# Optimization experiments

Hardware: AMD Instinct MI355X
Metric: run time of the kernel (lower is better)

## Reference

```python
import jax, jax.numpy as jnp
import numpy as np

N_POINTS = 1 << 20
N_LEVELS = 16
F_PER_LVL = 2
LOG2_T = 19
T = 1 << LOG2_T
BASE_RES = 16
PER_LEVEL_SCALE = float(np.exp2(np.log2(2048.0 / 16.0) / (N_LEVELS - 1)))
# 8 trilinear corner offsets [8,3]
OFFSETS = np.stack(np.meshgrid(*([np.array([0, 1])] * 3), indexing='ij'), axis=-1).reshape(8, 3)
PRIMES = np.array([1, 2654435761, 805459861], dtype=np.uint32)  # tcnn spatial hash primes


def _level_params(l):
    # tcnn: grid_scale = 2^(l*log2(s)) * base - 1 ; resolution = ceil(scale)+1
    scale = np.exp2(l * np.log2(PER_LEVEL_SCALE)) * BASE_RES - 1.0
    res = int(np.ceil(scale)) + 1
    return float(scale), res


def hash_encode(x, table):
    """x: [N,3] in [0,1]; table: [L,T,F]. Returns [N, L*F]."""
    offs = jnp.asarray(OFFSETS)                     # [8,3] int32
    primes = jnp.asarray(PRIMES)                    # [3] uint32
    feats = []
    for l in range(N_LEVELS):
        scale, res = _level_params(l)
        pos = x * scale + 0.5                       # [N,3]
        pos_grid = jnp.floor(pos)
        w = pos - pos_grid                          # [N,3] interp weights
        c0 = pos_grid.astype(jnp.int32)             # [N,3]
        corners = c0[None, :, :] + offs[:, None, :]  # [8,N,3]
        if res ** 3 <= T:
            # dense indexing for coarse levels (fits in hashmap)
            cc = jnp.clip(corners, 0, res - 1)
            idx = cc[..., 0] + cc[..., 1] * res + cc[..., 2] * (res * res)
        else:
            cu = corners.astype(jnp.uint32)
            h = (cu[..., 0] * primes[0]) ^ (cu[..., 1] * primes[1]) ^ (cu[..., 2] * primes[2])
            idx = (h & jnp.uint32(T - 1)).astype(jnp.int32)
        f = table[l][idx]                           # [8,N,F] gather
        # trilinear weights: prod over dims of (w if corner bit else 1-w)
        wc = jnp.prod(jnp.where(offs[:, None, :] == 1, w[None], 1.0 - w[None]), axis=-1)  # [8,N]
        feats.append(jnp.sum(wc[..., None] * f, axis=0))  # [N,F]
    return jnp.concatenate(feats, axis=-1)          # [N, 32]


def _softplus10(z):
    return jax.nn.softplus(10.0 * z) / 10.0


def setup_inputs() -> dict:
    key = jax.random.key(0)
    k = jax.random.split(key, 6)
    x = jax.random.uniform(k[0], (N_POINTS, 3), dtype=jnp.float32)
    table = jax.random.normal(k[1], (N_LEVELS, T, F_PER_LVL), dtype=jnp.float32) * 1e-2
    w1 = jax.random.normal(k[2], (64, 32), dtype=jnp.float32) * 0.1
    w2 = jax.random.normal(k[3], (64, 64), dtype=jnp.float32) * 0.1
    w3 = jax.random.normal(k[4], (64, 64), dtype=jnp.float32) * 0.1
    w4 = jax.random.normal(k[5], (1, 64), dtype=jnp.float32) * 0.1
    return {"x": x, "table": table, "w1": w1, "w2": w2, "w3": w3, "w4": w4}


def reference(x, table, w1, w2, w3, w4):
    enc = hash_encode(x, table)                     # [N,32]
    h = _softplus10(enc @ w1.T)
    h = _softplus10(h @ w2.T)
    h = _softplus10(h @ w3.T)
    sdf = h @ w4.T                                  # [N,1]
    return sdf
```

## Files before the change

kernel.cpp:

```cpp
#include <hip/hip_runtime.h>
#include <cmath>

#define T_SIZE (1u << 19)

typedef _Float16 h8 __attribute__((ext_vector_type(8)));
typedef _Float16 h4 __attribute__((ext_vector_type(4)));
typedef _Float16 h2 __attribute__((ext_vector_type(2)));
typedef float f4 __attribute__((ext_vector_type(4)));

struct Levels {
    float scale[16];
    int   res[16];
    unsigned dense_mask;
};

__device__ __forceinline__ float softplus10(float z) {
    float e = __builtin_amdgcn_exp2f(fminf(z * 14.426950408889634f, 126.0f));
    return __builtin_amdgcn_logf(1.0f + e) * 0.069314718055994531f;
}

__global__ __launch_bounds__(256) void convert_table_kernel(
    const float2* __restrict__ t, h2* __restrict__ o, int total4)
{
    int i = blockIdx.x * 256 + threadIdx.x;
    if (i >= total4) return;
    const float2* src = t + (size_t)i * 4;
    h8 r;
#pragma unroll
    for (int j = 0; j < 4; ++j) {
        float2 v = src[j];
        r[2 * j]     = (_Float16)v.x;
        r[2 * j + 1] = (_Float16)v.y;
    }
    *(h8*)(o + (size_t)i * 4) = r;
}

__global__ __launch_bounds__(256) void encode_kernel(
    const float* __restrict__ xs, const h2* __restrict__ table,
    h2* __restrict__ enc2, Levels lv, int N)
{
    __shared__ float sx[768];
    __shared__ float s_scale[16];
    __shared__ int   s_res[16];

    const int i0 = blockIdx.x * 256;
    for (int t = threadIdx.x; t < 768; t += 256) sx[t] = xs[(size_t)i0 * 3 + t];
    if (threadIdx.x < 16) {
        s_scale[threadIdx.x] = lv.scale[threadIdx.x];
        s_res[threadIdx.x]   = lv.res[threadIdx.x];
    }
    __syncthreads();

    const int l = blockIdx.y;
    const int i = i0 + threadIdx.x;
    if (i >= N) return;

    const float px = sx[threadIdx.x * 3 + 0];
    const float py = sx[threadIdx.x * 3 + 1];
    const float pz = sx[threadIdx.x * 3 + 2];
    const float s  = s_scale[l];
    const int  res = s_res[l];

    float fx = px * s + 0.5f, fy = py * s + 0.5f, fz = pz * s + 0.5f;
    float gx = floorf(fx), gy = floorf(fy), gz = floorf(fz);
    float wx = fx - gx, wy = fy - gy, wz = fz - gz;
    int cx = (int)gx, cy = (int)gy, cz = (int)gz;

    const h2* tl = table + (size_t)l * T_SIZE;
    float2 vx0[4], vx1[4];

    if ((lv.dense_mask >> l) & 1u) {
        int r1 = res - 1;
        int x0 = min(cx, r1), x1 = min(cx + 1, r1);
        int y0 = min(cy, r1), y1 = min(cy + 1, r1);
        int z0 = min(cz, r1), z1 = min(cz + 1, r1);
        int rr = res * res;
        int bases[4] = {y0 * res + z0 * rr, y0 * res + z1 * rr,
                        y1 * res + z0 * rr, y1 * res + z1 * rr};
#pragma unroll
        for (int j = 0; j < 4; ++j) {
            int idx0 = x0 + bases[j];
            int idx1 = x1 + bases[j];
            h4 pr = *(const h4*)(tl + (idx0 & ~1));
            float2 lo = make_float2((float)pr[0], (float)pr[1]);
            float2 hi = make_float2((float)pr[2], (float)pr[3]);
            bool hi0 = idx0 & 1;
            vx0[j] = hi0 ? hi : lo;
            if (hi0 && idx1 != idx0) {
                h2 v = tl[idx1];
                vx1[j] = make_float2((float)v[0], (float)v[1]);
            } else {
                vx1[j] = (idx1 == idx0) ? vx0[j] : hi;
            }
        }
    } else {
        unsigned hy0 = (unsigned)cy * 2654435761u, hy1 = (unsigned)(cy + 1) * 2654435761u;
        unsigned hz0 = (unsigned)cz * 805459861u,  hz1 = (unsigned)(cz + 1) * 805459861u;
        unsigned Y[4] = {hy0 ^ hz0, hy0 ^ hz1, hy1 ^ hz0, hy1 ^ hz1};
        const bool odd = (cx & 1);
        const unsigned M = T_SIZE - 1;
#pragma unroll
        for (int j = 0; j < 4; ++j) {
            unsigned h0m = ((unsigned)cx ^ Y[j]) & M;
            unsigned h1m = ((unsigned)(cx + 1) ^ Y[j]) & M;
            h4 pr = *(const h4*)(tl + (h0m & ~1u));
            float2 lo = make_float2((float)pr[0], (float)pr[1]);
            float2 hi = make_float2((float)pr[2], (float)pr[3]);
            bool h0hi = (h0m & 1u);
            vx0[j] = h0hi ? hi : lo;
            if (odd) {
                h2 v = tl[h1m];
                vx1[j] = make_float2((float)v[0], (float)v[1]);
            } else {
                vx1[j] = h0hi ? lo : hi;
            }
        }
    }

    float wx0 = 1.f - wx, wy0 = 1.f - wy, wz0 = 1.f - wz;
    float wyz[4] = {wy0 * wz0, wy0 * wz, wy * wz0, wy * wz};
    float f0 = 0.f, f1 = 0.f;
#pragma unroll
    for (int j = 0; j < 4; ++j) {
        float w0 = wx0 * wyz[j], w1 = wx * wyz[j];
        f0 += w0 * vx0[j].x + w1 * vx1[j].x;
        f1 += w0 * vx0[j].y + w1 * vx1[j].y;
    }

    h2 r;
    r[0] = (_Float16)f0;
    r[1] = (_Float16)f1;
    enc2[(size_t)l * N + i] = r;
}

__global__ __launch_bounds__(256, 3) void mlp_kernel(
    const h2* __restrict__ enc2,
    const float* __restrict__ w1, const float* __restrict__ w2,
    const float* __restrict__ w3, const float* __restrict__ w4,
    float* __restrict__ out, int nTiles, int N)
{
    constexpr int AR = 72;
    __shared__ __align__(16) _Float16 sAct[256 * AR];

    const int tid = threadIdx.x;
    const int wave = tid >> 6;
    const int lane = tid & 63;
    const int lrow = lane & 15;
    const int quad = lane >> 4;
    const int waveRow = wave * 64;
    const f4 zero = {0.f, 0.f, 0.f, 0.f};

    h8 aW1[4];
#pragma unroll
    for (int tm = 0; tm < 4; ++tm) {
        const float* src = w1 + (tm * 16 + lrow) * 32 + quad * 8;
#pragma unroll
        for (int j = 0; j < 8; ++j) aW1[tm][j] = (_Float16)src[j];
    }
    h8 aW2[4][2], aW3[4][2];
#pragma unroll
    for (int tm = 0; tm < 4; ++tm)
#pragma unroll
        for (int km = 0; km < 2; ++km) {
            const float* s2 = w2 + (tm * 16 + lrow) * 64 + km * 32 + quad * 8;
            const float* s3 = w3 + (tm * 16 + lrow) * 64 + km * 32 + quad * 8;
#pragma unroll
            for (int j = 0; j < 8; ++j) {
                aW2[tm][km][j] = (_Float16)s2[j];
                aW3[tm][km][j] = (_Float16)s3[j];
            }
        }
    float w4f[16];
#pragma unroll
    for (int tm = 0; tm < 4; ++tm)
#pragma unroll
        for (int r = 0; r < 4; ++r)
            w4f[tm * 4 + r] = w4[tm * 16 + quad * 4 + r];

    for (int tile = blockIdx.x; tile < nTiles; tile += gridDim.x) {
        const int blockPt = tile * 256;

#pragma unroll
        for (int t = 0; t < 4; ++t) {
            const int ptg = blockPt + waveRow + t * 16 + lrow;
            h8 b;
#pragma unroll
            for (int d = 0; d < 4; ++d) {
                h2 p = enc2[(size_t)(quad * 4 + d) * N + ptg];
                b[2 * d]     = p[0];
                b[2 * d + 1] = p[1];
            }
            const int arow = (waveRow + t * 16 + lrow) * AR;
#pragma unroll
            for (int tm = 0; tm < 4; ++tm) {
                f4 acc = __builtin_amdgcn_mfma_f32_16x16x32_f16(aW1[tm], b, zero, 0, 0, 0);
                h4 pk;
#pragma unroll
                for (int r = 0; r < 4; ++r) pk[r] = (_Float16)softplus10(acc[r]);
                *(h4*)&sAct[arow + tm * 16 + quad * 4] = pk;
            }
        }

#pragma unroll
        for (int t = 0; t < 4; ++t) {
            const int arow = (waveRow + t * 16 + lrow) * AR;
            h8 b0 = *(const h8*)&sAct[arow + quad * 8];
            h8 b1 = *(const h8*)&sAct[arow + 32 + quad * 8];
            f4 accs[4];
#pragma unroll
            for (int tm = 0; tm < 4; ++tm) {
                f4 acc = __builtin_amdgcn_mfma_f32_16x16x32_f16(aW2[tm][0], b0, zero, 0, 0, 0);
                acc     = __builtin_amdgcn_mfma_f32_16x16x32_f16(aW2[tm][1], b1, acc,  0, 0, 0);
                accs[tm] = acc;
            }
#pragma unroll
            for (int tm = 0; tm < 4; ++tm) {
                h4 pk;
#pragma unroll
                for (int r = 0; r < 4; ++r) pk[r] = (_Float16)softplus10(accs[tm][r]);
                *(h4*)&sAct[arow + tm * 16 + quad * 4] = pk;
            }
        }

#pragma unroll
        for (int t = 0; t < 4; ++t) {
            const int arow = (waveRow + t * 16 + lrow) * AR;
            h8 b0 = *(const h8*)&sAct[arow + quad * 8];
            h8 b1 = *(const h8*)&sAct[arow + 32 + quad * 8];
            float sum = 0.f;
#pragma unroll
            for (int tm = 0; tm < 4; ++tm) {
                f4 acc = __builtin_amdgcn_mfma_f32_16x16x32_f16(aW3[tm][0], b0, zero, 0, 0, 0);
                acc     = __builtin_amdgcn_mfma_f32_16x16x32_f16(aW3[tm][1], b1, acc,  0, 0, 0);
#pragma unroll
                for (int r = 0; r < 4; ++r)
                    sum += w4f[tm * 4 + r] * softplus10(acc[r]);
            }
            sum += __shfl_xor(sum, 16, 64);
            sum += __shfl_xor(sum, 32, 64);
            if (quad == 0)
                out[blockPt + waveRow + t * 16 + lrow] = sum;
        }
    }
}

__global__ __launch_bounds__(256) void encode_kernel_f32(
    const float* __restrict__ xs, const float2* __restrict__ table,
    h2* __restrict__ enc2, Levels lv, int N)
{
    const int i = blockIdx.x * 256 + threadIdx.x;
    const int l = blockIdx.y;
    if (i >= N) return;
    float px = xs[3 * i], py = xs[3 * i + 1], pz = xs[3 * i + 2];
    float s = lv.scale[l];
    int res = lv.res[l];
    float fx = px * s + 0.5f, fy = py * s + 0.5f, fz = pz * s + 0.5f;
    float gx = floorf(fx), gy = floorf(fy), gz = floorf(fz);
    float wx = fx - gx, wy = fy - gy, wz = fz - gz;
    int cx = (int)gx, cy = (int)gy, cz = (int)gz;
    unsigned idx[8];
    if ((lv.dense_mask >> l) & 1u) {
        int r1 = res - 1;
        int x0 = min(cx, r1), x1 = min(cx + 1, r1);
        int y0 = min(cy, r1), y1 = min(cy + 1, r1);
        int z0 = min(cz, r1), z1 = min(cz + 1, r1);
        int rr = res * res;
        idx[0] = x0 + y0 * res + z0 * rr; idx[1] = x0 + y0 * res + z1 * rr;
        idx[2] = x0 + y1 * res + z0 * rr; idx[3] = x0 + y1 * res + z1 * rr;
        idx[4] = x1 + y0 * res + z0 * rr; idx[5] = x1 + y0 * res + z1 * rr;
        idx[6] = x1 + y1 * res + z0 * rr; idx[7] = x1 + y1 * res + z1 * rr;
    } else {
        unsigned hx0 = (unsigned)cx, hx1 = (unsigned)(cx + 1);
        unsigned hy0 = (unsigned)cy * 2654435761u, hy1 = (unsigned)(cy + 1) * 2654435761u;
        unsigned hz0 = (unsigned)cz * 805459861u,  hz1 = (unsigned)(cz + 1) * 805459861u;
        idx[0] = (hx0^hy0^hz0) & (T_SIZE-1); idx[1] = (hx0^hy0^hz1) & (T_SIZE-1);
        idx[2] = (hx0^hy1^hz0) & (T_SIZE-1); idx[3] = (hx0^hy1^hz1) & (T_SIZE-1);
        idx[4] = (hx1^hy0^hz0) & (T_SIZE-1); idx[5] = (hx1^hy0^hz1) & (T_SIZE-1);
        idx[6] = (hx1^hy1^hz0) & (T_SIZE-1); idx[7] = (hx1^hy1^hz1) & (T_SIZE-1);
    }
    const float2* tl = table + (size_t)l * T_SIZE;
    float wx0 = 1.f - wx, wy0 = 1.f - wy, wz0 = 1.f - wz;
    float wcs[8] = {wx0*wy0*wz0, wx0*wy0*wz, wx0*wy*wz0, wx0*wy*wz,
                    wx*wy0*wz0,  wx*wy0*wz,  wx*wy*wz0,  wx*wy*wz};
    float f0 = 0.f, f1 = 0.f;
#pragma unroll
    for (int c = 0; c < 8; ++c) {
        float2 v = tl[idx[c]];
        f0 += wcs[c] * v.x; f1 += wcs[c] * v.y;
    }
    h2 r; r[0] = (_Float16)f0; r[1] = (_Float16)f1;
    enc2[(size_t)l * N + i] = r;
}

extern "C" void kernel_launch(void* const* d_in, const int* in_sizes, int n_in,
                              void* d_out, int out_size, void* d_ws, size_t ws_size,
                              hipStream_t stream) {
    const float* x     = (const float*)d_in[0];
    const float* table = (const float*)d_in[1];
    const float* w1    = (const float*)d_in[2];
    const float* w2    = (const float*)d_in[3];
    const float* w3    = (const float*)d_in[4];
    const float* w4    = (const float*)d_in[5];
    float* out = (float*)d_out;
    const int N = in_sizes[0] / 3;

    Levels lv;
    lv.dense_mask = 0;
    const double pls = exp2(log2(2048.0 / 16.0) / 15.0);
    const double lg  = log2(pls);
    for (int l = 0; l < 16; ++l) {
        double sc = exp2((double)l * lg) * 16.0 - 1.0;
        int res = (int)ceil(sc) + 1;
        lv.scale[l] = (float)sc;
        lv.res[l]   = res;
        if ((long long)res * res * res <= (long long)T_SIZE) lv.dense_mask |= (1u << l);
    }

    const size_t encBytes   = (size_t)16 * N * 4;
    const size_t tableBytes = (size_t)16 * T_SIZE * 4;
    h2* enc2 = (h2*)d_ws;

    const int ptBlocks = (N + 255) / 256;
    dim3 encGrid(ptBlocks, 16);

    if (ws_size >= encBytes + tableBytes) {
        h2* table16 = (h2*)((char*)d_ws + encBytes);
        const int total4 = 16 * T_SIZE / 4;
        hipLaunchKernelGGL(convert_table_kernel, dim3((total4 + 255) / 256), dim3(256), 0,
                           stream, (const float2*)table, table16, total4);
        hipLaunchKernelGGL(encode_kernel, encGrid, dim3(256), 0, stream,
                           x, (const h2*)table16, enc2, lv, N);
    } else {
        hipLaunchKernelGGL(encode_kernel_f32, encGrid, dim3(256), 0, stream,
                           x, (const float2*)table, enc2, lv, N);
    }

    const int nTiles = N / 256;
    const int mlpBlocks = 768;
    hipLaunchKernelGGL(mlp_kernel, dim3(mlpBlocks), dim3(256), 0, stream,
                       enc2, w1, w2, w3, w4, out, nTiles, N);
}
```

Baseline: 537.2 us.

## Interleave encoding by level groups, preconvert MLP weights to fp16, raise occupancy

The encoding buffer changes from level-major h2 to groups of four levels packed into 16-byte records per point. Each MLP lane now fetches its B fragment with a single 16-byte load instead of four strided 4-byte loads. A small kernel converts w1-w3 to fp16 once per call. The MLP kernel reloads W2 and W3 fragments inside its loop so fewer registers stay live, which allows launch bounds of 4 blocks per CU, and it switches from a grid-stride loop to fixed groups of 4 tiles per block. This assumes N is a multiple of 1024 and adds one extra launch plus repeated weight loads from cache.

```diff
diff --git a/kernel.cpp b/kernel.cpp
--- a/kernel.cpp
+++ b/kernel.cpp
@@ -35,9 +35,21 @@
     *(h8*)(o + (size_t)i * 4) = r;
 }
 
+__global__ __launch_bounds__(256) void convert_weights_kernel(
+    const float* __restrict__ w1, const float* __restrict__ w2,
+    const float* __restrict__ w3, _Float16* __restrict__ o)
+{
+    int i = blockIdx.x * 256 + threadIdx.x;
+    float v;
+    if (i < 2048)      v = w1[i];
+    else if (i < 6144) v = w2[i - 2048];
+    else               v = w3[i - 6144];
+    o[i] = (_Float16)v;
+}
+
 __global__ __launch_bounds__(256) void encode_kernel(
     const float* __restrict__ xs, const h2* __restrict__ table,
-    h2* __restrict__ enc2, Levels lv, int N)
+    char* __restrict__ enc3, Levels lv, int N)
 {
     __shared__ float sx[768];
     __shared__ float s_scale[16];
@@ -130,14 +142,27 @@
     h2 r;
     r[0] = (_Float16)f0;
     r[1] = (_Float16)f1;
-    enc2[(size_t)l * N + i] = r;
-}
-
-__global__ __launch_bounds__(256, 3) void mlp_kernel(
-    const h2* __restrict__ enc2,
-    const float* __restrict__ w1, const float* __restrict__ w2,
-    const float* __restrict__ w3, const float* __restrict__ w4,
-    float* __restrict__ out, int nTiles, int N)
+    *(h2*)(enc3 + (((size_t)(l >> 2) * N + i) << 4) + ((l & 3) << 2)) = r;
+}
+
+template <typename WT>
+__device__ __forceinline__ h8 load_frag8(const WT* p) {
+    if constexpr (sizeof(WT) == 2) {
+        return *(const h8*)p;
+    } else {
+        h8 r;
+#pragma unroll
+        for (int j = 0; j < 8; ++j) r[j] = (_Float16)p[j];
+        return r;
+    }
+}
+
+template <typename WT>
+__global__ __launch_bounds__(256, 4) void mlp_kernel(
+    const char* __restrict__ enc3,
+    const WT* __restrict__ w1, const WT* __restrict__ w2,
+    const WT* __restrict__ w3, const float* __restrict__ w4,
+    float* __restrict__ out, int N)
 {
     constexpr int AR = 72;
     __shared__ __align__(16) _Float16 sAct[256 * AR];
@@ -152,44 +177,33 @@
 
     h8 aW1[4];
 #pragma unroll
+    for (int tm = 0; tm < 4; ++tm)
+        aW1[tm] = load_frag8(w1 + (tm * 16 + lrow) * 32 + quad * 8);
+    h4 w4q[4];
+#pragma unroll
     for (int tm = 0; tm < 4; ++tm) {
-        const float* src = w1 + (tm * 16 + lrow) * 32 + quad * 8;
-#pragma unroll
-        for (int j = 0; j < 8; ++j) aW1[tm][j] = (_Float16)src[j];
-    }
-    h8 aW2[4][2], aW3[4][2];
-#pragma unroll
-    for (int tm = 0; tm < 4; ++tm)
-#pragma unroll
-        for (int km = 0; km < 2; ++km) {
-            const float* s2 = w2 + (tm * 16 + lrow) * 64 + km * 32 + quad * 8;
-            const float* s3 = w3 + (tm * 16 + lrow) * 64 + km * 32 + quad * 8;
-#pragma unroll
-            for (int j = 0; j < 8; ++j) {
-                aW2[tm][km][j] = (_Float16)s2[j];
-                aW3[tm][km][j] = (_Float16)s3[j];
-            }
-        }
-    float w4f[16];
-#pragma unroll
-    for (int tm = 0; tm < 4; ++tm)
-#pragma unroll
-        for (int r = 0; r < 4; ++r)
-            w4f[tm * 4 + r] = w4[tm * 16 + quad * 4 + r];
-
-    for (int tile = blockIdx.x; tile < nTiles; tile += gridDim.x) {
-        const int blockPt = tile * 256;
+        h4 t;
+#pragma unroll
+        for (int r = 0; r < 4; ++r) t[r] = (_Float16)w4[tm * 16 + quad * 4 + r];
+        w4q[tm] = t;
+    }
+
+#pragma unroll 1
+    for (int it = 0; it < 4; ++it) {
+        asm volatile("" ::: "memory");
+        h8 aW2[4][2];
+#pragma unroll
+        for (int tm = 0; tm < 4; ++tm)
+#pragma unroll
+            for (int km = 0; km < 2; ++km)
+                aW2[tm][km] = load_frag8(w2 + (tm * 16 + lrow) * 64 + km * 32 + quad * 8);
+
+        const int blockPt = (blockIdx.x * 4 + it) * 256;
 
 #pragma unroll
         for (int t = 0; t < 4; ++t) {
             const int ptg = blockPt + waveRow + t * 16 + lrow;
-            h8 b;
-#pragma unroll
-            for (int d = 0; d < 4; ++d) {
-                h2 p = enc2[(size_t)(quad * 4 + d) * N + ptg];
-                b[2 * d]     = p[0];
-                b[2 * d + 1] = p[1];
-            }
+            h8 b = *(const h8*)(enc3 + (((size_t)quad * N + ptg) << 4));
             const int arow = (waveRow + t * 16 + lrow) * AR;
 #pragma unroll
             for (int tm = 0; tm < 4; ++tm) {
@@ -222,6 +236,14 @@
             }
         }
 
+        asm volatile("" ::: "memory");
+        h8 aW3[4][2];
+#pragma unroll
+        for (int tm = 0; tm < 4; ++tm)
+#pragma unroll
+            for (int km = 0; km < 2; ++km)
+                aW3[tm][km] = load_frag8(w3 + (tm * 16 + lrow) * 64 + km * 32 + quad * 8);
+
 #pragma unroll
         for (int t = 0; t < 4; ++t) {
             const int arow = (waveRow + t * 16 + lrow) * AR;
@@ -234,7 +256,7 @@
                 acc     = __builtin_amdgcn_mfma_f32_16x16x32_f16(aW3[tm][1], b1, acc,  0, 0, 0);
 #pragma unroll
                 for (int r = 0; r < 4; ++r)
-                    sum += w4f[tm * 4 + r] * softplus10(acc[r]);
+                    sum += (float)w4q[tm][r] * softplus10(acc[r]);
             }
             sum += __shfl_xor(sum, 16, 64);
             sum += __shfl_xor(sum, 32, 64);
@@ -246,7 +268,7 @@
 
 __global__ __launch_bounds__(256) void encode_kernel_f32(
     const float* __restrict__ xs, const float2* __restrict__ table,
-    h2* __restrict__ enc2, Levels lv, int N)
+    char* __restrict__ enc3, Levels lv, int N)
 {
     const int i = blockIdx.x * 256 + threadIdx.x;
     const int l = blockIdx.y;
@@ -289,7 +311,7 @@
         f0 += wcs[c] * v.x; f1 += wcs[c] * v.y;
     }
     h2 r; r[0] = (_Float16)f0; r[1] = (_Float16)f1;
-    enc2[(size_t)l * N + i] = r;
+    *(h2*)(enc3 + (((size_t)(l >> 2) * N + i) << 4) + ((l & 3) << 2)) = r;
 }
 
 extern "C" void kernel_launch(void* const* d_in, const int* in_sizes, int n_in,
@@ -318,25 +340,29 @@
 
     const size_t encBytes   = (size_t)16 * N * 4;
     const size_t tableBytes = (size_t)16 * T_SIZE * 4;
-    h2* enc2 = (h2*)d_ws;
+    const size_t whBytes    = 32768;
+    char* enc3 = (char*)d_ws;
 
     const int ptBlocks = (N + 255) / 256;
     dim3 encGrid(ptBlocks, 16);
-
-    if (ws_size >= encBytes + tableBytes) {
+    const int mlpBlocks = N / (256 * 4);
+
+    if (ws_size >= encBytes + tableBytes + whBytes) {
         h2* table16 = (h2*)((char*)d_ws + encBytes);
+        _Float16* wh = (_Float16*)((char*)d_ws + encBytes + tableBytes);
         const int total4 = 16 * T_SIZE / 4;
         hipLaunchKernelGGL(convert_table_kernel, dim3((total4 + 255) / 256), dim3(256), 0,
                            stream, (const float2*)table, table16, total4);
+        hipLaunchKernelGGL(convert_weights_kernel, dim3(40), dim3(256), 0, stream,
+                           w1, w2, w3, wh);
         hipLaunchKernelGGL(encode_kernel, encGrid, dim3(256), 0, stream,
-                           x, (const h2*)table16, enc2, lv, N);
+                           x, (const h2*)table16, enc3, lv, N);
+        hipLaunchKernelGGL((mlp_kernel<_Float16>), dim3(mlpBlocks), dim3(256), 0, stream,
+                           enc3, wh, wh + 2048, wh + 6144, w4, out, N);
     } else {
         hipLaunchKernelGGL(encode_kernel_f32, encGrid, dim3(256), 0, stream,
-                           x, (const float2*)table, enc2, lv, N);
-    }
-
-    const int nTiles = N / 256;
-    const int mlpBlocks = 768;
-    hipLaunchKernelGGL(mlp_kernel, dim3(mlpBlocks), dim3(256), 0, stream,
-                       enc2, w1, w2, w3, w4, out, nTiles, N);
-}
+                           x, (const float2*)table, enc3, lv, N);
+        hipLaunchKernelGGL((mlp_kernel<float>), dim3(mlpBlocks), dim3(256), 0, stream,
+                           enc3, w1, w2, w3, w4, out, N);
+    }
+}
```

Result: slower. 550.6 us (+2.5%).

## Gather corner pairs with 16-byte loads, split encode into level groups, pre-convert weights

Applied to the files above, without the earlier changes.

Corner-pair gathers now load a 16-byte aligned group of four fp16 entries and pull the second corner from it when it falls in the same group. This replaces the 8-byte load that only covered the neighbour when the first index was even. The encode launch is split into four launches of four levels each, probably to keep each group's table slices resident in cache. MLP weights are converted to fp16 once in a small kernel, so each MLP block loads fp16 fragments directly instead of converting fp32 values per thread. The changes add extra kernel launches, and the wider gather loads fetch more bytes per access.

```diff
diff --git a/kernel.cpp b/kernel.cpp
--- a/kernel.cpp
+++ b/kernel.cpp
@@ -35,9 +35,47 @@
     *(h8*)(o + (size_t)i * 4) = r;
 }
 
+__global__ __launch_bounds__(256) void convert_weights_kernel(
+    const float* __restrict__ w1, const float* __restrict__ w2,
+    const float* __restrict__ w3, _Float16* __restrict__ o)
+{
+    int i = blockIdx.x * 256 + threadIdx.x;
+    float v;
+    if (i < 2048)      v = w1[i];
+    else if (i < 6144) v = w2[i - 2048];
+    else               v = w3[i - 6144];
+    o[i] = (_Float16)v;
+}
+
+__device__ __forceinline__ void gather_pair(
+    const h2* __restrict__ tl, unsigned i0, unsigned i1,
+    float2& v0, float2& v1)
+{
+    unsigned g = i0 & ~3u;
+    union { h8 v; uint4 u; } cv;
+    cv.v = *(const h8*)(tl + g);
+    unsigned p0 = i0 & 3u;
+    unsigned a01 = (p0 & 1u) ? cv.u.y : cv.u.x;
+    unsigned a23 = (p0 & 1u) ? cv.u.w : cv.u.z;
+    unsigned e0  = (p0 & 2u) ? a23 : a01;
+    unsigned e1;
+    if ((i1 & ~3u) == g) {
+        unsigned p1 = i1 & 3u;
+        unsigned b01 = (p1 & 1u) ? cv.u.y : cv.u.x;
+        unsigned b23 = (p1 & 1u) ? cv.u.w : cv.u.z;
+        e1 = (p1 & 2u) ? b23 : b01;
+    } else {
+        e1 = *(const unsigned*)(tl + i1);
+    }
+    h2 c0 = __builtin_bit_cast(h2, e0);
+    h2 c1 = __builtin_bit_cast(h2, e1);
+    v0 = make_float2((float)c0[0], (float)c0[1]);
+    v1 = make_float2((float)c1[0], (float)c1[1]);
+}
+
 __global__ __launch_bounds__(256) void encode_kernel(
     const float* __restrict__ xs, const h2* __restrict__ table,
-    h2* __restrict__ enc2, Levels lv, int N)
+    h2* __restrict__ enc2, Levels lv, int lbase, int N)
 {
     __shared__ float sx[768];
     __shared__ float s_scale[16];
@@ -51,7 +89,7 @@
     }
     __syncthreads();
 
-    const int l = blockIdx.y;
+    const int l = lbase + blockIdx.y;
     const int i = i0 + threadIdx.x;
     if (i >= N) return;
 
@@ -78,43 +116,18 @@
         int bases[4] = {y0 * res + z0 * rr, y0 * res + z1 * rr,
                         y1 * res + z0 * rr, y1 * res + z1 * rr};
 #pragma unroll
-        for (int j = 0; j < 4; ++j) {
-            int idx0 = x0 + bases[j];
-            int idx1 = x1 + bases[j];
-            h4 pr = *(const h4*)(tl + (idx0 & ~1));
-            float2 lo = make_float2((float)pr[0], (float)pr[1]);
-            float2 hi = make_float2((float)pr[2], (float)pr[3]);
-            bool hi0 = idx0 & 1;
-            vx0[j] = hi0 ? hi : lo;
-            if (hi0 && idx1 != idx0) {
-                h2 v = tl[idx1];
-                vx1[j] = make_float2((float)v[0], (float)v[1]);
-            } else {
-                vx1[j] = (idx1 == idx0) ? vx0[j] : hi;
-            }
-        }
+        for (int j = 0; j < 4; ++j)
+            gather_pair(tl, (unsigned)(x0 + bases[j]), (unsigned)(x1 + bases[j]),
+                        vx0[j], vx1[j]);
     } else {
         unsigned hy0 = (unsigned)cy * 2654435761u, hy1 = (unsigned)(cy + 1) * 2654435761u;
         unsigned hz0 = (unsigned)cz * 805459861u,  hz1 = (unsigned)(cz + 1) * 805459861u;
         unsigned Y[4] = {hy0 ^ hz0, hy0 ^ hz1, hy1 ^ hz0, hy1 ^ hz1};
-        const bool odd = (cx & 1);
         const unsigned M = T_SIZE - 1;
 #pragma unroll
-        for (int j = 0; j < 4; ++j) {
-            unsigned h0m = ((unsigned)cx ^ Y[j]) & M;
-            unsigned h1m = ((unsigned)(cx + 1) ^ Y[j]) & M;
-            h4 pr = *(const h4*)(tl + (h0m & ~1u));
-            float2 lo = make_float2((float)pr[0], (float)pr[1]);
-            float2 hi = make_float2((float)pr[2], (float)pr[3]);
-            bool h0hi = (h0m & 1u);
-            vx0[j] = h0hi ? hi : lo;
-            if (odd) {
-                h2 v = tl[h1m];
-                vx1[j] = make_float2((float)v[0], (float)v[1]);
-            } else {
-                vx1[j] = h0hi ? lo : hi;
-            }
-        }
+        for (int j = 0; j < 4; ++j)
+            gather_pair(tl, ((unsigned)cx ^ Y[j]) & M,
+                        ((unsigned)(cx + 1) ^ Y[j]) & M, vx0[j], vx1[j]);
     }
 
     float wx0 = 1.f - wx, wy0 = 1.f - wy, wz0 = 1.f - wz;
@@ -133,10 +146,23 @@
     enc2[(size_t)l * N + i] = r;
 }
 
+template <typename WT>
+__device__ __forceinline__ h8 load_frag8(const WT* p) {
+    if constexpr (sizeof(WT) == 2) {
+        return *(const h8*)p;
+    } else {
+        h8 r;
+#pragma unroll
+        for (int j = 0; j < 8; ++j) r[j] = (_Float16)p[j];
+        return r;
+    }
+}
+
+template <typename WT>
 __global__ __launch_bounds__(256, 3) void mlp_kernel(
     const h2* __restrict__ enc2,
-    const float* __restrict__ w1, const float* __restrict__ w2,
-    const float* __restrict__ w3, const float* __restrict__ w4,
+    const WT* __restrict__ w1, const WT* __restrict__ w2,
+    const WT* __restrict__ w3, const float* __restrict__ w4,
     float* __restrict__ out, int nTiles, int N)
 {
     constexpr int AR = 72;
@@ -152,23 +178,15 @@
 
     h8 aW1[4];
 #pragma unroll
-    for (int tm = 0; tm < 4; ++tm) {
-        const float* src = w1 + (tm * 16 + lrow) * 32 + quad * 8;
-#pragma unroll
-        for (int j = 0; j < 8; ++j) aW1[tm][j] = (_Float16)src[j];
-    }
+    for (int tm = 0; tm < 4; ++tm)
+        aW1[tm] = load_frag8(w1 + (tm * 16 + lrow) * 32 + quad * 8);
     h8 aW2[4][2], aW3[4][2];
 #pragma unroll
     for (int tm = 0; tm < 4; ++tm)
 #pragma unroll
         for (int km = 0; km < 2; ++km) {
-            const float* s2 = w2 + (tm * 16 + lrow) * 64 + km * 32 + quad * 8;
-            const float* s3 = w3 + (tm * 16 + lrow) * 64 + km * 32 + quad * 8;
-#pragma unroll
-            for (int j = 0; j < 8; ++j) {
-                aW2[tm][km][j] = (_Float16)s2[j];
-                aW3[tm][km][j] = (_Float16)s3[j];
-            }
+            aW2[tm][km] = load_frag8(w2 + (tm * 16 + lrow) * 64 + km * 32 + quad * 8);
+            aW3[tm][km] = load_frag8(w3 + (tm * 16 + lrow) * 64 + km * 32 + quad * 8);
         }
     float w4f[16];
 #pragma unroll
@@ -318,25 +336,30 @@
 
     const size_t encBytes   = (size_t)16 * N * 4;
     const size_t tableBytes = (size_t)16 * T_SIZE * 4;
+    const size_t whBytes    = 32768;
     h2* enc2 = (h2*)d_ws;
 
     const int ptBlocks = (N + 255) / 256;
-    dim3 encGrid(ptBlocks, 16);
-
-    if (ws_size >= encBytes + tableBytes) {
+    const int nTiles = N / 256;
+    const int mlpBlocks = 768;
+
+    if (ws_size >= encBytes + tableBytes + whBytes) {
         h2* table16 = (h2*)((char*)d_ws + encBytes);
+        _Float16* wh = (_Float16*)((char*)d_ws + encBytes + tableBytes);
         const int total4 = 16 * T_SIZE / 4;
         hipLaunchKernelGGL(convert_table_kernel, dim3((total4 + 255) / 256), dim3(256), 0,
                            stream, (const float2*)table, table16, total4);
-        hipLaunchKernelGGL(encode_kernel, encGrid, dim3(256), 0, stream,
-                           x, (const h2*)table16, enc2, lv, N);
-    } else {
-        hipLaunchKernelGGL(encode_kernel_f32, encGrid, dim3(256), 0, stream,
+        hipLaunchKernelGGL(convert_weights_kernel, dim3(40), dim3(256), 0, stream,
+                           w1, w2, w3, wh);
+        for (int lbase = 0; lbase < 16; lbase += 4)
+            hipLaunchKernelGGL(encode_kernel, dim3(ptBlocks, 4), dim3(256), 0, stream,
+                               x, (const h2*)table16, enc2, lv, lbase, N);
+        hipLaunchKernelGGL((mlp_kernel<_Float16>), dim3(mlpBlocks), dim3(256), 0, stream,
+                           enc2, wh, wh + 2048, wh + 6144, w4, out, nTiles, N);
+    } else {
+        hipLaunchKernelGGL(encode_kernel_f32, dim3(ptBlocks, 16), dim3(256), 0, stream,
                            x, (const float2*)table, enc2, lv, N);
-    }
-
-    const int nTiles = N / 256;
-    const int mlpBlocks = 768;
-    hipLaunchKernelGGL(mlp_kernel, dim3(mlpBlocks), dim3(256), 0, stream,
-                       enc2, w1, w2, w3, w4, out, nTiles, N);
-}
+        hipLaunchKernelGGL((mlp_kernel<float>), dim3(mlpBlocks), dim3(256), 0, stream,
+                           enc2, w1, w2, w3, w4, out, nTiles, N);
+    }
+}
```

Result: faster. 455.2 us (-15.3%).
